# Performance work log

Measured on AMD Instinct MI355X. Metric: run time of the kernel, lower is better.

Reference implementation:

```python
import jax, jax.numpy as jnp
import numpy as np
from jax import lax

D_MODEL, D_INNER, D_STATE, D_CONV, DT_RANK = 128, 256, 16, 4, 8
BATCH, SEQ = 8, 4096


def setup_inputs() -> dict:
    key = jax.random.key(0)
    ks = jax.random.split(key, 13)
    g = lambda k, shape, fan: (jax.random.normal(k, shape, jnp.float32) / np.sqrt(fan)).astype(jnp.float32)
    inp = {
        "s": jax.random.normal(ks[0], (BATCH, SEQ, D_MODEL), jnp.float32),
        "in_proj_w": g(ks[1], (2 * D_INNER, D_MODEL), D_MODEL),
        "conv_w": g(ks[2], (D_INNER, 1, D_CONV), D_CONV),
        "conv_b": jnp.zeros((D_INNER,), jnp.float32),
        "x_proj_w": g(ks[3], (DT_RANK + 2 * D_STATE, D_INNER), D_INNER),
        "dt_proj_w": g(ks[4], (D_INNER, DT_RANK), DT_RANK),
        "dt_proj_b": jax.random.uniform(ks[5], (D_INNER,), jnp.float32, -4.0, -2.0),  # softplus(b) small, like mamba dt init
        "A_log": jnp.log(jnp.broadcast_to(jnp.arange(1, D_STATE + 1, dtype=jnp.float32), (D_INNER, D_STATE))),
        "D_skip": jnp.ones((D_INNER,), jnp.float32),
        "out_proj_w": g(ks[6], (D_MODEL, D_INNER), D_INNER),
        "ln_gamma": jnp.ones((D_MODEL,), jnp.float32),
        "ln_beta": jnp.zeros((D_MODEL,), jnp.float32),
        "fc_w": g(ks[7], (D_MODEL, D_MODEL), D_MODEL),
    }
    return inp


def _mamba(s, in_proj_w, conv_w, conv_b, x_proj_w, dt_proj_w, dt_proj_b, A_log, D_skip, out_proj_w):
    B, L, _ = s.shape
    xz = jnp.einsum("bld,ed->ble", s, in_proj_w)           # [B,L,2*D_INNER]
    x, z = jnp.split(xz, 2, axis=-1)                        # each [B,L,D_INNER]
    # causal depthwise conv1d
    xc = jnp.transpose(x, (0, 2, 1))                        # [B,D_INNER,L]
    xc = jnp.pad(xc, ((0, 0), (0, 0), (D_CONV - 1, 0)))
    xc = lax.conv_general_dilated(xc, conv_w, (1,), "VALID",
                                  dimension_numbers=("NCH", "OIH", "NCH"),
                                  feature_group_count=D_INNER)
    x = jax.nn.silu(jnp.transpose(xc + conv_b[None, :, None], (0, 2, 1)))  # [B,L,D_INNER]
    # input-dependent dt, B, C
    x_dbl = jnp.einsum("bld,ed->ble", x, x_proj_w)
    dt = x_dbl[..., :DT_RANK]
    Bc = x_dbl[..., DT_RANK:DT_RANK + D_STATE]              # [B,L,D_STATE]
    Cc = x_dbl[..., DT_RANK + D_STATE:]                     # [B,L,D_STATE]
    dt = jax.nn.softplus(jnp.einsum("blr,dr->bld", dt, dt_proj_w) + dt_proj_b)  # [B,L,D_INNER]
    A = -jnp.exp(A_log)                                     # [D_INNER,D_STATE]

    def step(h, inp):
        dt_t, b_t, c_t, u_t = inp                           # [B,Di],[B,Ds],[B,Ds],[B,Di]
        dA = jnp.exp(dt_t[:, :, None] * A)                  # [B,Di,Ds]
        dBu = (dt_t * u_t)[:, :, None] * b_t[:, None, :]
        h = dA * h + dBu
        y = jnp.einsum("bds,bs->bd", h, c_t)
        return h, y

    h0 = jnp.zeros((B, D_INNER, D_STATE), x.dtype)
    xs = (jnp.swapaxes(dt, 0, 1), jnp.swapaxes(Bc, 0, 1), jnp.swapaxes(Cc, 0, 1), jnp.swapaxes(x, 0, 1))
    _, ys = lax.scan(step, h0, xs)                          # ys: [L,B,D_INNER]
    y = jnp.swapaxes(ys, 0, 1) + x * D_skip
    y = y * jax.nn.silu(z)
    return jnp.einsum("bld,od->blo", y, out_proj_w)         # [B,L,D_MODEL]


def reference(s, in_proj_w, conv_w, conv_b, x_proj_w, dt_proj_w, dt_proj_b, A_log, D_skip, out_proj_w, ln_gamma, ln_beta, fc_w):
    h = _mamba(s, in_proj_w, conv_w, conv_b, x_proj_w, dt_proj_w, dt_proj_b, A_log, D_skip, out_proj_w)
    mu = jnp.mean(h, axis=-1, keepdims=True)
    var = jnp.mean(jnp.square(h - mu), axis=-1, keepdims=True)
    hn = (h - mu) * lax.rsqrt(var + 1e-5) * ln_gamma + ln_beta
    return jax.nn.relu(jnp.einsum("bld,od->blo", hn, fc_w))
```

## Files before the change

kernel.cpp:

```cpp
#include <hip/hip_runtime.h>
#include <math.h>

#define B_ 8
#define L_ 4096
#define DM 128
#define DI 256
#define DSN 16
#define RK 8
#define M_ (B_*L_)
#define NC 128
#define CH 32
#define CH2 64

typedef __attribute__((ext_vector_type(8))) short bfrag;
typedef __attribute__((ext_vector_type(4))) float ffrag;
typedef __attribute__((ext_vector_type(2))) float f32x2;

__device__ __forceinline__ float silu_f(float x) {
  return x * __builtin_amdgcn_rcpf(1.f + __expf(-x));
}
__device__ __forceinline__ float softplus_f(float x) {
  return (x > 20.f) ? x : __logf(1.f + __expf(x));
}

__device__ __forceinline__ unsigned short f2bf(float f) {
  unsigned int u = __builtin_bit_cast(unsigned int, f);
  unsigned int r = (u + 0x7FFFu + ((u >> 16) & 1u)) >> 16;
  return (unsigned short)r;
}
__device__ __forceinline__ unsigned int f2bf2(float lo, float hi) {
  return (unsigned int)f2bf(lo) | ((unsigned int)f2bf(hi) << 16);
}
__device__ __forceinline__ float bf2f(unsigned int us) {
  return __builtin_bit_cast(float, us << 16);
}

__global__ __launch_bounds__(256)
void prep_weights(const float* __restrict__ w_in, const float* __restrict__ xw,
                  const float* __restrict__ ow, const float* __restrict__ fcw,
                  unsigned short* __restrict__ w_in_b, unsigned short* __restrict__ xw_b,
                  unsigned short* __restrict__ ow_b, unsigned short* __restrict__ fcw_b) {
  const int i = blockIdx.x * 256 + threadIdx.x;
  const float* src; unsigned short* dst; int j;
  if (i < 16384)      { src = w_in; dst = w_in_b; j = i; }
  else if (i < 18944) { src = xw;   dst = xw_b;   j = i - 16384; }
  else if (i < 27136) { src = ow;   dst = ow_b;   j = i - 18944; }
  else if (i < 31232) { src = fcw;  dst = fcw_b;  j = i - 27136; }
  else return;
  float4 v = *(const float4*)&src[j << 2];
  uint2 p = {f2bf2(v.x, v.y), f2bf2(v.z, v.w)};
  *(uint2*)&dst[j << 2] = p;
}

__global__ __launch_bounds__(512, 4)
void xproj_dtproj(const float* __restrict__ s, const unsigned short* __restrict__ w_in_b,
                  const unsigned short* __restrict__ xw_b,
                  const float* __restrict__ dtw, const float* __restrict__ dtpb,
                  const float* __restrict__ cw, const float* __restrict__ cb,
                  const float* __restrict__ alog,
                  float* __restrict__ Bb, float* __restrict__ Cb,
                  unsigned int* __restrict__ udt,
                  unsigned short* __restrict__ zsb,
                  unsigned short* __restrict__ cP, unsigned short* __restrict__ cHe) {
  __shared__ __align__(16) char pool[76336];
  unsigned short* As = (unsigned short*)pool;
  unsigned short* ua = (unsigned short*)pool;
  unsigned short* hx = (unsigned short*)(pool + 33792);
  unsigned short* wb = (unsigned short*)(pool + 33792);
  float* dtr_s = (float*)(pool + 69168);
  float* Bs_l  = (float*)(pool + 72240);
  const int t = threadIdx.x;
  const int p0 = blockIdx.x << 6;
  const int w = t >> 6, l = t & 63, q = l >> 4, col = l & 15;

  for (int i = t; i < 80 * 32; i += 512) {
    int row = i >> 5, c4 = i & 31;
    int pos = (row < 64) ? (p0 + row) : (p0 - 16 + (row - 64));
    if (pos < 0) pos = 0;
    float4 av = *(const float4*)&s[pos * 128 + (c4 << 2)];
    uint2 ap = {f2bf2(av.x, av.y), f2bf2(av.z, av.w)};
    *(uint2*)&As[row * 136 + (c4 << 2)] = ap;
  }
  __syncthreads();
  for (int jt = 0; jt < 8; ++jt) {
    const int wrow0 = jt << 6;
    const int T = (jt < 4) ? 20 : 16;
    for (int tile = w; tile < T; tile += 8) {
      const int mt = tile >> 2, nt = tile & 3;
      ffrag acc = {0.f, 0.f, 0.f, 0.f};
#pragma unroll
      for (int s8 = 0; s8 < 4; ++s8) {
        int k0 = s8 * 32 + q * 8;
        bfrag af = *(const bfrag*)&As[((mt << 4) + col) * 136 + k0];
        bfrag wf = *(const bfrag*)&w_in_b[(wrow0 + (nt << 4) + col) * 128 + k0];
        acc = __builtin_amdgcn_mfma_f32_16x16x32_bf16(wf, af, acc, 0, 0, 0);
      }
      const int chb = (nt << 4) + (q << 2);
      if (jt < 4) {
        uint2 pk = {f2bf2(acc[0], acc[1]), f2bf2(acc[2], acc[3])};
        const int ch = (jt << 6) + chb;
        if (mt < 4) {
          *(uint2*)&hx[(3 + (mt << 4) + col) * 264 + ch] = pk;
        } else if (col >= 13) {
          *(uint2*)&hx[(col - 13) * 264 + ch] = pk;
        }
      } else {
        uint2 pk = {f2bf2(silu_f(acc[0]), silu_f(acc[1])),
                    f2bf2(silu_f(acc[2]), silu_f(acc[3]))};
        const int m = p0 + (mt << 4) + col;
        *(uint2*)&zsb[m * 256 + ((jt - 4) << 6) + chb] = pk;
      }
    }
  }
  __syncthreads();
  {
    const int k = t & 255, half = t >> 8;
    const int pstart = half << 5;
    const int base = p0 + pstart;
    const int lb = base & (L_ - 1);
    const float w0 = cw[k*4], w1 = cw[k*4+1], w2 = cw[k*4+2], w3 = cw[k*4+3];
    const float bias = cb[k];
    float x0 = (lb >= 3) ? bf2f((unsigned int)hx[(pstart + 0) * 264 + k]) : 0.f;
    float x1 = (lb >= 2) ? bf2f((unsigned int)hx[(pstart + 1) * 264 + k]) : 0.f;
    float x2 = (lb >= 1) ? bf2f((unsigned int)hx[(pstart + 2) * 264 + k]) : 0.f;
#pragma unroll 8
    for (int it = 0; it < 32; ++it) {
      float x3 = bf2f((unsigned int)hx[(pstart + 3 + it) * 264 + k]);
      float u = silu_f(fmaf(w0, x0, fmaf(w1, x1, fmaf(w2, x2, fmaf(w3, x3, bias)))));
      ua[(pstart + it) * 264 + k] = f2bf(u);
      x0 = x1; x1 = x2; x2 = x3;
    }
  }
  __syncthreads();
  for (int i = t; i < 40 * 32; i += 512) {
    int row = i >> 5, c8 = (i & 31) << 3;
    *(uint4*)&wb[row * 264 + c8] = *(const uint4*)&xw_b[row * 256 + c8];
  }
  for (int i = t; i < 8 * 264; i += 512) wb[40 * 264 + i] = 0;
  __syncthreads();
  for (int tile = w; tile < 12; tile += 8) {
    const int mt = tile & 3, nt = tile >> 2;
    ffrag acc = {0.f, 0.f, 0.f, 0.f};
#pragma unroll
    for (int s8 = 0; s8 < 8; ++s8) {
      int k0 = s8 * 32 + q * 8;
      bfrag af = *(const bfrag*)&ua[((mt << 4) + col) * 264 + k0];
      bfrag wf = *(const bfrag*)&wb[((nt << 4) + col) * 264 + k0];
      acc = __builtin_amdgcn_mfma_f32_16x16x32_bf16(wf, af, acc, 0, 0, 0);
    }
    const int ml = (mt << 4) + col;
    const int m = p0 + ml;
    const int n0 = (nt << 4) + (q << 2);
    float4 v = {acc[0], acc[1], acc[2], acc[3]};
    if (n0 < 8) {
      *(float4*)&dtr_s[ml * 12 + n0] = v;
    } else if (n0 < 24) {
      *(float4*)&Bb[m * 16 + (n0 - 8)] = v;
      *(float4*)&Bs_l[ml * 16 + (n0 - 8)] = v;
    } else if (n0 < 40) {
      *(float4*)&Cb[m * 16 + (n0 - 24)] = v;
    }
  }
  __syncthreads();
  {
    const int d = t & 255, half = t >> 8;
    const int pstart = half << 5;
    const int gpos = p0 + pstart;
    const int bb = gpos >> 12;
    const int cc = (gpos & (L_ - 1)) >> 5;
    const int bc = bb * NC + cc;
    float w8[8];
    *(float4*)&w8[0] = *(const float4*)&dtw[d * 8];
    *(float4*)&w8[4] = *(const float4*)&dtw[d * 8 + 4];
    const float bias = dtpb[d];
    float a[16];
    bool okl = true;
#pragma unroll
    for (int j = 0; j < 16; ++j) {
      a[j] = -__expf(alog[d * 16 + j]);
      float tgt = (float)(j + 1);
      okl = okl && (fabsf(a[j] + tgt) <= 1e-3f * tgt);
    }
    const bool fast = (bool)__all((int)okl);
    f32x2 h2[8] = {{0.f,0.f},{0.f,0.f},{0.f,0.f},{0.f,0.f},
                   {0.f,0.f},{0.f,0.f},{0.f,0.f},{0.f,0.f}};
    float sdt = 0.f;
#pragma unroll 2
    for (int pp = pstart; pp < pstart + 32; ++pp) {
      float r0[8];
      *(float4*)&r0[0] = *(const float4*)&dtr_s[pp * 12];
      *(float4*)&r0[4] = *(const float4*)&dtr_s[pp * 12 + 4];
      float a2 = bias;
#pragma unroll
      for (int r2 = 0; r2 < 8; ++r2) a2 = fmaf(r0[r2], w8[r2], a2);
      float sp = softplus_f(a2);
      unsigned int uq = (unsigned int)ua[pp * 264 + d];
      unsigned short spb = f2bf(sp);
      udt[(p0 + pp) * 256 + d] = uq | ((unsigned int)spb << 16);
      float dtv = bf2f((unsigned int)spb);
      float uv  = bf2f(uq);
      float du = dtv * uv;
      sdt += dtv;
      const float* brow = &Bs_l[pp * 16];
      float4 b0 = *(const float4*)&brow[0];
      float4 b1 = *(const float4*)&brow[4];
      float4 b2 = *(const float4*)&brow[8];
      float4 b3 = *(const float4*)&brow[12];
      f32x2 B2[8] = {{b0.x,b0.y},{b0.z,b0.w},{b1.x,b1.y},{b1.z,b1.w},
                     {b2.x,b2.y},{b2.z,b2.w},{b3.x,b3.y},{b3.z,b3.w}};
      f32x2 du2 = {du, du};
      if (fast) {
        float e1 = __expf(-dtv);
        float e2 = e1 * e1;
        f32x2 dA = {e1, e2};
        f32x2 e22 = {e2, e2};
#pragma unroll
        for (int jj = 0; jj < 8; ++jj) {
          h2[jj] = dA * h2[jj] + du2 * B2[jj];
          dA = dA * e22;
        }
      } else {
#pragma unroll
        for (int j = 0; j < 16; ++j) {
          float dA = __expf(dtv * a[j]);
          h2[j >> 1][j & 1] = fmaf(dA, h2[j >> 1][j & 1], du * B2[j >> 1][j & 1]);
        }
      }
    }
#pragma unroll
    for (int j = 0; j < 16; ++j) {
      int o = (bc * 16 + j) * 256 + d;
      cP[o]  = f2bf(__expf(a[j] * sdt));
      cHe[o] = f2bf(h2[j >> 1][j & 1]);
    }
  }
}

__global__ __launch_bounds__(512)
void scan_combine(unsigned short* __restrict__ cP, const unsigned short* __restrict__ cHe) {
  __shared__ float segP[64 * 9], segH[64 * 9], segS[64 * 9];
  const int t = threadIdx.x;
  const int sdl = t & 63, seg = t >> 6;
  const int blk = blockIdx.x;
  const int b = blk >> 6, grp = blk & 63;
  const int sd = (grp << 6) + sdl;
  const int base = b * NC * 4096 + sd;
  float Pacc = 1.f, Hacc = 0.f;
#pragma unroll
  for (int i = 0; i < 16; ++i) {
    int idx = base + (seg * 16 + i) * 4096;
    float p = bf2f((unsigned int)cP[idx]);
    float he = bf2f((unsigned int)cHe[idx]);
    Hacc = fmaf(p, Hacc, he);
    Pacc *= p;
  }
  segP[sdl * 9 + seg] = Pacc;
  segH[sdl * 9 + seg] = Hacc;
  __syncthreads();
  if (t < 64) {
    float hs = 0.f;
#pragma unroll
    for (int s2 = 0; s2 < 8; ++s2) {
      segS[t * 9 + s2] = hs;
      hs = fmaf(segP[t * 9 + s2], hs, segH[t * 9 + s2]);
    }
  }
  __syncthreads();
  float hs = segS[sdl * 9 + seg];
#pragma unroll
  for (int i = 0; i < 16; ++i) {
    int idx = base + (seg * 16 + i) * 4096;
    float p = bf2f((unsigned int)cP[idx]);
    float he = bf2f((unsigned int)cHe[idx]);
    cP[idx] = f2bf(hs);
    hs = fmaf(p, hs, he);
  }
}

__global__ __launch_bounds__(512, 4)
void scan3_out_ln_fc(const unsigned int* __restrict__ udt,
                     const float* __restrict__ Bb, const float* __restrict__ Cb,
                     const float* __restrict__ alog, const unsigned short* __restrict__ hst,
                     const float* __restrict__ dsk,
                     const unsigned short* __restrict__ zsb,
                     const unsigned short* __restrict__ ow_b,
                     const float* __restrict__ gamma, const float* __restrict__ beta,
                     const unsigned short* __restrict__ fcw_b, float* __restrict__ out) {
  __shared__ float Bs[CH2 * 16];
  __shared__ float Cs[CH2 * 16];
  __shared__ unsigned short smA[64 * 264];
  __shared__ unsigned short smB[128 * 136];
  const int bc = blockIdx.x;
  const int b = bc >> 6, cc = bc & 63;
  const int t = threadIdx.x;
  const int l = t & 63, w = t >> 6;
  const int chh = t >> 8;
  const int d = t & 255;
  const int base = b * L_ + (cc << 1) * CH;
  const int cbase = base + chh * CH;
  const int hc = b * NC + (cc << 1) + chh;
  if (t < CH2 * 4)           ((float4*)Bs)[t]            = *(const float4*)&Bb[base * 16 + (t << 2)];
  else if (t < CH2 * 8)      ((float4*)Cs)[t - CH2 * 4]  = *(const float4*)&Cb[base * 16 + ((t - CH2 * 4) << 2)];
  float a[16];
  bool okl = true;
#pragma unroll
  for (int j = 0; j < 16; ++j) {
    a[j] = -__expf(alog[d * 16 + j]);
    float tgt = (float)(j + 1);
    okl = okl && (fabsf(a[j] + tgt) <= 1e-3f * tgt);
  }
  const bool fast = (bool)__all((int)okl);
  const float dskv = dsk[d];
  f32x2 h2[8];
#pragma unroll
  for (int jj = 0; jj < 8; ++jj) {
    h2[jj][0] = bf2f((unsigned int)hst[(hc * 16 + (jj << 1)) * 256 + d]);
    h2[jj][1] = bf2f((unsigned int)hst[(hc * 16 + (jj << 1) + 1) * 256 + d]);
  }
  unsigned int wv0 = udt[cbase * 256 + d];
  unsigned int wv1 = udt[(cbase + 1) * 256 + d];
  unsigned short zv0 = zsb[cbase * 256 + d];
  unsigned short zv1 = zsb[(cbase + 1) * 256 + d];
  __syncthreads();
#pragma unroll 2
  for (int ll = 0; ll < CH; ++ll) {
    const int l2 = (ll + 2 < CH) ? ll + 2 : CH - 1;
    unsigned int wv2 = udt[(cbase + l2) * 256 + d];
    unsigned short zv2 = zsb[(cbase + l2) * 256 + d];
    const float* brow = &Bs[(chh * CH + ll) * 16];
    const float* crow = &Cs[(chh * CH + ll) * 16];
    float4 b0 = *(const float4*)&brow[0];
    float4 b1 = *(const float4*)&brow[4];
    float4 b2 = *(const float4*)&brow[8];
    float4 b3 = *(const float4*)&brow[12];
    float4 c0 = *(const float4*)&crow[0];
    float4 c1 = *(const float4*)&crow[4];
    float4 c2 = *(const float4*)&crow[8];
    float4 c3 = *(const float4*)&crow[12];
    float uv  = bf2f(wv0 & 0xFFFFu);
    float dtv = bf2f(wv0 >> 16);
    f32x2 B2[8] = {{b0.x,b0.y},{b0.z,b0.w},{b1.x,b1.y},{b1.z,b1.w},
                   {b2.x,b2.y},{b2.z,b2.w},{b3.x,b3.y},{b3.z,b3.w}};
    f32x2 C2[8] = {{c0.x,c0.y},{c0.z,c0.w},{c1.x,c1.y},{c1.z,c1.w},
                   {c2.x,c2.y},{c2.z,c2.w},{c3.x,c3.y},{c3.z,c3.w}};
    float du = dtv * uv;
    f32x2 du2 = {du, du};
    f32x2 y2 = {0.f, 0.f};
    if (fast) {
      float e1 = __expf(-dtv);
      float e2 = e1 * e1;
      f32x2 dA = {e1, e2};
      f32x2 e22 = {e2, e2};
#pragma unroll
      for (int jj = 0; jj < 8; ++jj) {
        h2[jj] = dA * h2[jj] + du2 * B2[jj];
        y2 = y2 + h2[jj] * C2[jj];
        dA = dA * e22;
      }
    } else {
#pragma unroll
      for (int j = 0; j < 16; ++j) {
        float dA = __expf(dtv * a[j]);
        float hh = fmaf(dA, h2[j >> 1][j & 1], du * B2[j >> 1][j & 1]);
        h2[j >> 1][j & 1] = hh;
        y2[j & 1] = fmaf(hh, C2[j >> 1][j & 1], y2[j & 1]);
      }
    }
    float y = y2.x + y2.y;
    float zs = bf2f((unsigned int)zv0);
    smA[(chh * CH + ll) * 264 + d] = f2bf(fmaf(uv, dskv, y) * zs);
    wv0 = wv1; wv1 = wv2; zv0 = zv1; zv1 = zv2;
  }
  const int q = l >> 4, col = l & 15;
  ffrag acc[2][4];
  for (int nt2 = 0; nt2 < 2; ++nt2) {
    __syncthreads();
    for (int i = t; i < 64 * 32; i += 512) {
      int row = i >> 5, c8 = (i & 31) << 3;
      *(uint4*)&smB[row * 264 + c8] = *(const uint4*)&ow_b[((nt2 << 6) + row) * 256 + c8];
    }
    __syncthreads();
    if (t < 256) {
#pragma unroll
      for (int nt = 0; nt < 4; ++nt) acc[nt2][nt] = (ffrag){0.f, 0.f, 0.f, 0.f};
#pragma unroll
      for (int s8 = 0; s8 < 8; ++s8) {
        int k0 = s8 * 32 + q * 8;
        bfrag af = *(const bfrag*)&smA[((w << 4) + col) * 264 + k0];
#pragma unroll
        for (int nt = 0; nt < 4; ++nt) {
          bfrag bf_ = *(const bfrag*)&smB[((nt << 4) + col) * 264 + k0];
          acc[nt2][nt] = __builtin_amdgcn_mfma_f32_16x16x32_bf16(af, bf_, acc[nt2][nt], 0, 0, 0);
        }
      }
    }
  }
  float mu[4], rs[4];
  if (t < 256) {
#pragma unroll
    for (int i = 0; i < 4; ++i) {
      float s1 = 0.f, s2 = 0.f;
#pragma unroll
      for (int nt2 = 0; nt2 < 2; ++nt2)
#pragma unroll
        for (int nt = 0; nt < 4; ++nt) {
          float v = acc[nt2][nt][i];
          s1 += v; s2 = fmaf(v, v, s2);
        }
      s1 += __shfl_xor(s1, 1); s2 += __shfl_xor(s2, 1);
      s1 += __shfl_xor(s1, 2); s2 += __shfl_xor(s2, 2);
      s1 += __shfl_xor(s1, 4); s2 += __shfl_xor(s2, 4);
      s1 += __shfl_xor(s1, 8); s2 += __shfl_xor(s2, 8);
      mu[i] = s1 * (1.f / DM);
      float var = s2 * (1.f / DM) - mu[i] * mu[i];
      rs[i] = rsqrtf(var + 1e-5f);
    }
  }
  __syncthreads();
  if (t < 256) {
#pragma unroll
    for (int nt2 = 0; nt2 < 2; ++nt2)
#pragma unroll
      for (int nt = 0; nt < 4; ++nt) {
        int n = (nt2 << 6) + (nt << 4) + col;
        float g = gamma[n], be = beta[n];
#pragma unroll
        for (int i = 0; i < 4; ++i) {
          int r = (w << 4) + (q << 2) + i;
          smA[r * 136 + n] = f2bf(fmaf((acc[nt2][nt][i] - mu[i]) * rs[i], g, be));
        }
      }
  }
  for (int i = t; i < 128 * 16; i += 512) {
    int row = i >> 4, c8 = (i & 15) << 3;
    *(uint4*)&smB[row * 136 + c8] = *(const uint4*)&fcw_b[row * 128 + c8];
  }
  __syncthreads();
  if (t < 256) {
    ffrag a2[8] = {{0.f,0.f,0.f,0.f},{0.f,0.f,0.f,0.f},{0.f,0.f,0.f,0.f},{0.f,0.f,0.f,0.f},
                   {0.f,0.f,0.f,0.f},{0.f,0.f,0.f,0.f},{0.f,0.f,0.f,0.f},{0.f,0.f,0.f,0.f}};
#pragma unroll
    for (int s8 = 0; s8 < 4; ++s8) {
      int k0 = s8 * 32 + q * 8;
      bfrag af = *(const bfrag*)&smA[((w << 4) + col) * 136 + k0];
#pragma unroll
      for (int nt = 0; nt < 8; ++nt) {
        bfrag bf_ = *(const bfrag*)&smB[((nt << 4) + col) * 136 + k0];
        a2[nt] = __builtin_amdgcn_mfma_f32_16x16x32_bf16(af, bf_, a2[nt], 0, 0, 0);
      }
    }
#pragma unroll
    for (int nt = 0; nt < 8; ++nt)
#pragma unroll
      for (int i = 0; i < 4; ++i) {
        int ml = (w << 4) + (q << 2) + i;
        out[(base + ml) * 128 + (nt << 4) + col] = fmaxf(a2[nt][i], 0.f);
      }
  }
}

extern "C" void kernel_launch(void* const* d_in, const int* in_sizes, int n_in,
                              void* d_out, int out_size, void* d_ws, size_t ws_size,
                              hipStream_t stream) {
  (void)in_sizes; (void)n_in; (void)out_size; (void)ws_size;
  const float* s    = (const float*)d_in[0];
  const float* w_in = (const float*)d_in[1];
  const float* cw   = (const float*)d_in[2];
  const float* cb   = (const float*)d_in[3];
  const float* xw   = (const float*)d_in[4];
  const float* dtw  = (const float*)d_in[5];
  const float* dtpb = (const float*)d_in[6];
  const float* alog = (const float*)d_in[7];
  const float* dsk  = (const float*)d_in[8];
  const float* ow   = (const float*)d_in[9];
  const float* gam  = (const float*)d_in[10];
  const float* bet  = (const float*)d_in[11];
  const float* fcw  = (const float*)d_in[12];
  float* out = (float*)d_out;
  float* ws  = (float*)d_ws;

  unsigned short* zsb  = (unsigned short*)(ws + 4194304);
  unsigned int*   udt  = (unsigned int*)(ws + 8388608);
  float*          Bb   = ws + 16777216;
  float*          Cb   = ws + 17301504;
  unsigned short* cP   = (unsigned short*)(ws + 17825792);
  unsigned short* cHe  = (unsigned short*)(ws + 19922944);
  unsigned short* w_in_b = (unsigned short*)(ws + 22020096);
  unsigned short* xw_b   = (unsigned short*)(ws + 22052864);
  unsigned short* ow_b   = (unsigned short*)(ws + 22057984);
  unsigned short* fcw_b  = (unsigned short*)(ws + 22074368);

  prep_weights<<<122, 256, 0, stream>>>(w_in, xw, ow, fcw, w_in_b, xw_b, ow_b, fcw_b);
  xproj_dtproj<<<512, 512, 0, stream>>>(s, w_in_b, xw_b, dtw, dtpb, cw, cb, alog,
                                        Bb, Cb, udt, zsb, cP, cHe);
  scan_combine<<<512, 512, 0, stream>>>(cP, cHe);
  scan3_out_ln_fc<<<B_ * NC / 2, 512, 0, stream>>>(udt, Bb, Cb, alog, cP, dsk, zsb,
                                                   ow_b, gam, bet, fcw_b, out);
}
```

Baseline: 167.1 us.

## Halve xproj block tile, read projection weights directly from global memory

The xproj_dtproj kernel now processes 32 positions per block with 256 threads instead of 64 with 512, which roughly halves its shared memory and doubles the grid. The x_proj weights are no longer staged into LDS; MFMA operands are loaded straight from global (cache-resident) memory with zero padding for rows past 40. In the final kernel, the out_proj and fc weights are also read directly from global rather than through the smB staging buffer, which removes that buffer and several syncthreads. The aim is more resident blocks and less staging and sync overhead, at the cost of more global and cache traffic per MFMA, a larger halo overhead per position, and redundant weight reads across waves.

```diff
diff --git a/kernel.cpp b/kernel.cpp
--- a/kernel.cpp
+++ b/kernel.cpp
@@ -52,7 +52,7 @@
   *(uint2*)&dst[j << 2] = p;
 }
 
-__global__ __launch_bounds__(512, 4)
+__global__ __launch_bounds__(256, 4)
 void xproj_dtproj(const float* __restrict__ s, const unsigned short* __restrict__ w_in_b,
                   const unsigned short* __restrict__ xw_b,
                   const float* __restrict__ dtw, const float* __restrict__ dtpb,
@@ -62,20 +62,19 @@
                   unsigned int* __restrict__ udt,
                   unsigned short* __restrict__ zsb,
                   unsigned short* __restrict__ cP, unsigned short* __restrict__ cHe) {
-  __shared__ __align__(16) char pool[76336];
+  __shared__ __align__(16) char pool[38960];
   unsigned short* As = (unsigned short*)pool;
   unsigned short* ua = (unsigned short*)pool;
-  unsigned short* hx = (unsigned short*)(pool + 33792);
-  unsigned short* wb = (unsigned short*)(pool + 33792);
-  float* dtr_s = (float*)(pool + 69168);
-  float* Bs_l  = (float*)(pool + 72240);
+  unsigned short* hx = (unsigned short*)(pool + 16896);
+  float* dtr_s = (float*)(pool + 35376);
+  float* Bs_l  = (float*)(pool + 36912);
   const int t = threadIdx.x;
-  const int p0 = blockIdx.x << 6;
+  const int p0 = blockIdx.x << 5;
   const int w = t >> 6, l = t & 63, q = l >> 4, col = l & 15;
 
-  for (int i = t; i < 80 * 32; i += 512) {
+  for (int i = t; i < 48 * 32; i += 256) {
     int row = i >> 5, c4 = i & 31;
-    int pos = (row < 64) ? (p0 + row) : (p0 - 16 + (row - 64));
+    int pos = (row < 32) ? (p0 + row) : (p0 - 16 + (row - 32));
     if (pos < 0) pos = 0;
     float4 av = *(const float4*)&s[pos * 128 + (c4 << 2)];
     uint2 ap = {f2bf2(av.x, av.y), f2bf2(av.z, av.w)};
@@ -84,8 +83,8 @@
   __syncthreads();
   for (int jt = 0; jt < 8; ++jt) {
     const int wrow0 = jt << 6;
-    const int T = (jt < 4) ? 20 : 16;
-    for (int tile = w; tile < T; tile += 8) {
+    const int T = (jt < 4) ? 12 : 8;
+    for (int tile = w; tile < T; tile += 4) {
       const int mt = tile >> 2, nt = tile & 3;
       ffrag acc = {0.f, 0.f, 0.f, 0.f};
 #pragma unroll
@@ -99,7 +98,7 @@
       if (jt < 4) {
         uint2 pk = {f2bf2(acc[0], acc[1]), f2bf2(acc[2], acc[3])};
         const int ch = (jt << 6) + chb;
-        if (mt < 4) {
+        if (mt < 2) {
           *(uint2*)&hx[(3 + (mt << 4) + col) * 264 + ch] = pk;
         } else if (col >= 13) {
           *(uint2*)&hx[(col - 13) * 264 + ch] = pk;
@@ -114,38 +113,32 @@
   }
   __syncthreads();
   {
-    const int k = t & 255, half = t >> 8;
-    const int pstart = half << 5;
-    const int base = p0 + pstart;
-    const int lb = base & (L_ - 1);
+    const int k = t;
+    const int lb = p0 & (L_ - 1);
     const float w0 = cw[k*4], w1 = cw[k*4+1], w2 = cw[k*4+2], w3 = cw[k*4+3];
     const float bias = cb[k];
-    float x0 = (lb >= 3) ? bf2f((unsigned int)hx[(pstart + 0) * 264 + k]) : 0.f;
-    float x1 = (lb >= 2) ? bf2f((unsigned int)hx[(pstart + 1) * 264 + k]) : 0.f;
-    float x2 = (lb >= 1) ? bf2f((unsigned int)hx[(pstart + 2) * 264 + k]) : 0.f;
+    float x0 = (lb >= 3) ? bf2f((unsigned int)hx[0 * 264 + k]) : 0.f;
+    float x1 = (lb >= 2) ? bf2f((unsigned int)hx[1 * 264 + k]) : 0.f;
+    float x2 = (lb >= 1) ? bf2f((unsigned int)hx[2 * 264 + k]) : 0.f;
 #pragma unroll 8
     for (int it = 0; it < 32; ++it) {
-      float x3 = bf2f((unsigned int)hx[(pstart + 3 + it) * 264 + k]);
+      float x3 = bf2f((unsigned int)hx[(3 + it) * 264 + k]);
       float u = silu_f(fmaf(w0, x0, fmaf(w1, x1, fmaf(w2, x2, fmaf(w3, x3, bias)))));
-      ua[(pstart + it) * 264 + k] = f2bf(u);
+      ua[it * 264 + k] = f2bf(u);
       x0 = x1; x1 = x2; x2 = x3;
     }
   }
   __syncthreads();
-  for (int i = t; i < 40 * 32; i += 512) {
-    int row = i >> 5, c8 = (i & 31) << 3;
-    *(uint4*)&wb[row * 264 + c8] = *(const uint4*)&xw_b[row * 256 + c8];
-  }
-  for (int i = t; i < 8 * 264; i += 512) wb[40 * 264 + i] = 0;
-  __syncthreads();
-  for (int tile = w; tile < 12; tile += 8) {
-    const int mt = tile & 3, nt = tile >> 2;
+  for (int tile = w; tile < 6; tile += 4) {
+    const int mt = tile & 1, nt = tile >> 1;
     ffrag acc = {0.f, 0.f, 0.f, 0.f};
 #pragma unroll
     for (int s8 = 0; s8 < 8; ++s8) {
       int k0 = s8 * 32 + q * 8;
       bfrag af = *(const bfrag*)&ua[((mt << 4) + col) * 264 + k0];
-      bfrag wf = *(const bfrag*)&wb[((nt << 4) + col) * 264 + k0];
+      const int nrow = (nt << 4) + col;
+      bfrag wf = {0, 0, 0, 0, 0, 0, 0, 0};
+      if (nrow < 40) wf = *(const bfrag*)&xw_b[nrow * 256 + k0];
       acc = __builtin_amdgcn_mfma_f32_16x16x32_bf16(wf, af, acc, 0, 0, 0);
     }
     const int ml = (mt << 4) + col;
@@ -163,11 +156,9 @@
   }
   __syncthreads();
   {
-    const int d = t & 255, half = t >> 8;
-    const int pstart = half << 5;
-    const int gpos = p0 + pstart;
-    const int bb = gpos >> 12;
-    const int cc = (gpos & (L_ - 1)) >> 5;
+    const int d = t;
+    const int bb = p0 >> 12;
+    const int cc = (p0 & (L_ - 1)) >> 5;
     const int bc = bb * NC + cc;
     float w8[8];
     *(float4*)&w8[0] = *(const float4*)&dtw[d * 8];
@@ -186,7 +177,7 @@
                    {0.f,0.f},{0.f,0.f},{0.f,0.f},{0.f,0.f}};
     float sdt = 0.f;
 #pragma unroll 2
-    for (int pp = pstart; pp < pstart + 32; ++pp) {
+    for (int pp = 0; pp < 32; ++pp) {
       float r0[8];
       *(float4*)&r0[0] = *(const float4*)&dtr_s[pp * 12];
       *(float4*)&r0[4] = *(const float4*)&dtr_s[pp * 12 + 4];
@@ -289,7 +280,6 @@
   __shared__ float Bs[CH2 * 16];
   __shared__ float Cs[CH2 * 16];
   __shared__ unsigned short smA[64 * 264];
-  __shared__ unsigned short smB[128 * 136];
   const int bc = blockIdx.x;
   const int b = bc >> 6, cc = bc & 63;
   const int t = threadIdx.x;
@@ -373,30 +363,25 @@
   }
   const int q = l >> 4, col = l & 15;
   ffrag acc[2][4];
-  for (int nt2 = 0; nt2 < 2; ++nt2) {
-    __syncthreads();
-    for (int i = t; i < 64 * 32; i += 512) {
-      int row = i >> 5, c8 = (i & 31) << 3;
-      *(uint4*)&smB[row * 264 + c8] = *(const uint4*)&ow_b[((nt2 << 6) + row) * 256 + c8];
-    }
-    __syncthreads();
-    if (t < 256) {
+  float mu[4], rs[4];
+  __syncthreads();
+  if (t < 256) {
+#pragma unroll
+    for (int nt2 = 0; nt2 < 2; ++nt2)
 #pragma unroll
       for (int nt = 0; nt < 4; ++nt) acc[nt2][nt] = (ffrag){0.f, 0.f, 0.f, 0.f};
 #pragma unroll
-      for (int s8 = 0; s8 < 8; ++s8) {
-        int k0 = s8 * 32 + q * 8;
-        bfrag af = *(const bfrag*)&smA[((w << 4) + col) * 264 + k0];
+    for (int s8 = 0; s8 < 8; ++s8) {
+      int k0 = s8 * 32 + q * 8;
+      bfrag af = *(const bfrag*)&smA[((w << 4) + col) * 264 + k0];
+#pragma unroll
+      for (int nt2 = 0; nt2 < 2; ++nt2)
 #pragma unroll
         for (int nt = 0; nt < 4; ++nt) {
-          bfrag bf_ = *(const bfrag*)&smB[((nt << 4) + col) * 264 + k0];
-          acc[nt2][nt] = __builtin_amdgcn_mfma_f32_16x16x32_bf16(af, bf_, acc[nt2][nt], 0, 0, 0);
-        }
-      }
-    }
-  }
-  float mu[4], rs[4];
-  if (t < 256) {
+          bfrag wf = *(const bfrag*)&ow_b[((nt2 << 6) + (nt << 4) + col) * 256 + k0];
+          acc[nt2][nt] = __builtin_amdgcn_mfma_f32_16x16x32_bf16(af, wf, acc[nt2][nt], 0, 0, 0);
+        }
+    }
 #pragma unroll
     for (int i = 0; i < 4; ++i) {
       float s1 = 0.f, s2 = 0.f;
@@ -431,10 +416,6 @@
         }
       }
   }
-  for (int i = t; i < 128 * 16; i += 512) {
-    int row = i >> 4, c8 = (i & 15) << 3;
-    *(uint4*)&smB[row * 136 + c8] = *(const uint4*)&fcw_b[row * 128 + c8];
-  }
   __syncthreads();
   if (t < 256) {
     ffrag a2[8] = {{0.f,0.f,0.f,0.f},{0.f,0.f,0.f,0.f},{0.f,0.f,0.f,0.f},{0.f,0.f,0.f,0.f},
@@ -445,8 +426,8 @@
       bfrag af = *(const bfrag*)&smA[((w << 4) + col) * 136 + k0];
 #pragma unroll
       for (int nt = 0; nt < 8; ++nt) {
-        bfrag bf_ = *(const bfrag*)&smB[((nt << 4) + col) * 136 + k0];
-        a2[nt] = __builtin_amdgcn_mfma_f32_16x16x32_bf16(af, bf_, a2[nt], 0, 0, 0);
+        bfrag wf = *(const bfrag*)&fcw_b[((nt << 4) + col) * 128 + k0];
+        a2[nt] = __builtin_amdgcn_mfma_f32_16x16x32_bf16(af, wf, a2[nt], 0, 0, 0);
       }
     }
 #pragma unroll
@@ -491,8 +472,8 @@
   unsigned short* fcw_b  = (unsigned short*)(ws + 22074368);
 
   prep_weights<<<122, 256, 0, stream>>>(w_in, xw, ow, fcw, w_in_b, xw_b, ow_b, fcw_b);
-  xproj_dtproj<<<512, 512, 0, stream>>>(s, w_in_b, xw_b, dtw, dtpb, cw, cb, alog,
-                                        Bb, Cb, udt, zsb, cP, cHe);
+  xproj_dtproj<<<M_ / CH, 256, 0, stream>>>(s, w_in_b, xw_b, dtw, dtpb, cw, cb, alog,
+                                            Bb, Cb, udt, zsb, cP, cHe);
   scan_combine<<<512, 512, 0, stream>>>(cP, cHe);
   scan3_out_ln_fc<<<B_ * NC / 2, 512, 0, stream>>>(udt, Bb, Cb, alog, cP, dsk, zsb,
                                                    ow_b, gam, bet, fcw_b, out);
```

New measurement: 177.1 us. 6.0% more time.
